# Optimization experiments

Hardware: AMD Instinct MI355X
Metric: run time of the kernel (lower is better)

## Reference

```python
import jax, jax.numpy as jnp
import numpy as np

EMBED = 1152
HEADS = 16
HEAD_DIM = EMBED // HEADS
SCALE = HEAD_DIM ** -0.5


def setup_inputs() -> dict:
    key = jax.random.key(0)
    k1, k2, k3, k4, k5 = jax.random.split(key, 5)
    B, S = 32, 729
    std = EMBED ** -0.5
    return {
        "hidden_state": jax.random.normal(k1, (B, S, EMBED), dtype=jnp.float32),
        "qkv_w": jax.random.normal(k2, (3 * EMBED, EMBED), dtype=jnp.float32) * std,
        "qkv_b": jax.random.normal(k3, (3 * EMBED,), dtype=jnp.float32) * 0.02,
        "out_w": jax.random.normal(k4, (EMBED, EMBED), dtype=jnp.float32) * std,
        "out_b": jax.random.normal(k5, (EMBED,), dtype=jnp.float32) * 0.02,
    }


def reference(hidden_state, qkv_w, qkv_b, out_w, out_b):
    B, S, _ = hidden_state.shape
    qkv = hidden_state @ qkv_w.T + qkv_b  # [B,S,3E]
    q, k, v = jnp.split(qkv, 3, axis=-1)
    # [B,S,E] -> [B,H,S,Dh]
    def heads(x):
        return x.reshape(B, S, HEADS, HEAD_DIM).transpose(0, 2, 1, 3)
    q, k, v = heads(q), heads(k), heads(v)
    scores = jnp.einsum("bhqd,bhkd->bhqk", q, k) * SCALE
    scores = jax.nn.softmax(scores, axis=-1)  # [B,H,S,S]
    out = jnp.einsum("bhqk,bhkd->bhqd", scores, v)
    out = out.transpose(0, 2, 1, 3).reshape(B, S, EMBED)
    out = out @ out_w.T + out_b
    return out, scores
```

## Files before the change

### kernel.cpp

```cpp
#include <hip/hip_runtime.h>

#define B_    32
#define S_    729
#define E_    1152
#define H_    16
#define D_    72
#define M1_   23328
#define MPAD_ 23424
#define SQ_   736
#define SK_   768
#define DP_   96
#define VR_   96
#define SCALE_ 0.11785113019775793f

typedef __attribute__((ext_vector_type(8))) _Float16 f16x8;
typedef __attribute__((ext_vector_type(4))) _Float16 f16x4;
typedef __attribute__((ext_vector_type(4))) float    f32x4;

#define GLDS16(g, l) __builtin_amdgcn_global_load_lds(                      \
    (__attribute__((address_space(1))) void*)(g),                           \
    (__attribute__((address_space(3))) void*)(l), 16, 0, 0)

union H2U { _Float16 h[2]; uint32_t u; };

__global__ void cvt_f16(const float4* __restrict__ src, f16x4* __restrict__ dst, int n4) {
  int stride = gridDim.x * blockDim.x;
  for (int i = blockIdx.x * blockDim.x + threadIdx.x; i < n4; i += stride) {
    float4 v = src[i];
    f16x4 o;
    o.x = (_Float16)v.x; o.y = (_Float16)v.y;
    o.z = (_Float16)v.z; o.w = (_Float16)v.w;
    dst[i] = o;
  }
}

template<int MODE>
__global__ __launch_bounds__(256)
void gemm_f16(const _Float16* __restrict__ A, const _Float16* __restrict__ W,
              const float* __restrict__ bias,
              _Float16* __restrict__ Qp, _Float16* __restrict__ Kp,
              _Float16* __restrict__ Vtp, float* __restrict__ Cout)
{
  __shared__ _Float16 As[128 * 64];
  __shared__ _Float16 Bs[128 * 64];
  const int tid = threadIdx.x;
  const int l  = tid & 63;
  const int wv = tid >> 6;
  const int lq = l & 15, lk = l >> 4;
  const int m0 = blockIdx.x * 128;
  const int n0 = blockIdx.y * 128;
  const int wm = (wv & 1) * 64, wn = (wv >> 1) * 64;
  const int srow = l >> 3;
  const int scol = (l & 7) * 8;

  f32x4 acc[4][4] = {};

  for (int k0 = 0; k0 < 1152; k0 += 64) {
    #pragma unroll
    for (int q = 0; q < 4; ++q) {
      int chunk = wv * 4 + q;
      int row = chunk * 8 + srow;
      GLDS16(A + (size_t)(m0 + row) * 1152 + k0 + scol, &As[chunk * 512 + l * 8]);
      GLDS16(W + (size_t)(n0 + row) * 1152 + k0 + scol, &Bs[chunk * 512 + l * 8]);
    }
    __syncthreads();
    #pragma unroll
    for (int kk = 0; kk < 64; kk += 32) {
      f16x8 a[4], b[4];
      #pragma unroll
      for (int i = 0; i < 4; ++i)
        a[i] = *(const f16x8*)&As[(wm + 16 * i + lq) * 64 + kk + lk * 8];
      #pragma unroll
      for (int j = 0; j < 4; ++j)
        b[j] = *(const f16x8*)&Bs[(wn + 16 * j + lq) * 64 + kk + lk * 8];
      #pragma unroll
      for (int i = 0; i < 4; ++i)
        #pragma unroll
        for (int j = 0; j < 4; ++j)
          acc[i][j] = __builtin_amdgcn_mfma_f32_16x16x32_f16(a[i], b[j], acc[i][j], 0, 0, 0);
    }
    __syncthreads();
  }

  #pragma unroll
  for (int i = 0; i < 4; ++i) {
    #pragma unroll
    for (int j = 0; j < 4; ++j) {
      int n = n0 + wn + 16 * j + lq;
      float bn = bias[n];
      #pragma unroll
      for (int r = 0; r < 4; ++r) {
        int m = m0 + wm + 16 * i + lk * 4 + r;
        if (m >= M1_) continue;
        float v = acc[i][j][r] + bn;
        if (MODE == 0) {
          unsigned um = (unsigned)m;
          unsigned bq = um / 729u, s = um - bq * 729u;
          unsigned un = (unsigned)n;
          unsigned which = un / 1152u, e = un - which * 1152u;
          unsigned h = e / 72u, d = e - h * 72u;
          unsigned bh = bq * 16u + h;
          if (which == 0) {
            Qp[((size_t)bh * SQ_ + s) * DP_ + d] = (_Float16)(v * SCALE_);
          } else if (which == 1) {
            Kp[((size_t)bh * SK_ + s) * DP_ + d] = (_Float16)v;
          } else {
            Vtp[((size_t)bh * VR_ + d) * 768 + s] = (_Float16)v;
          }
        } else {
          Cout[(size_t)m * 1152 + n] = v;
        }
      }
    }
  }
}

struct AttnSmem {
  union {
    char  stage[2][24576];
    float ored[4][32][96];
  };
  uint32_t pexch[8][64][4];
  float redmax[32][4];
  float redsum[32][4];
  float invl[32];
};

__global__ __launch_bounds__(512, 4)
void attn_k(const _Float16* __restrict__ Q, const _Float16* __restrict__ K,
            const _Float16* __restrict__ Vt, float* __restrict__ scores,
            _Float16* __restrict__ AO)
{
  __shared__ AttnSmem sm;
  const int tid = threadIdx.x;
  const int l   = tid & 63;
  const int wv  = tid >> 6;
  const int lq  = l & 15, lk = l >> 4;
  const int i   = wv >> 2;
  const int sl  = wv & 3;
  const int p    = blockIdx.x;
  const int xcd  = p & 7;
  const int slot = p >> 3;
  const int hl   = slot / 23;
  const int qt   = slot - hl * 23;
  const int bh   = hl * 8 + xcd;
  const int q0   = qt * 32;
  const int b    = bh >> 4, h = bh & 15;

  const _Float16* Qb = Q  + (size_t)bh * SQ_ * DP_;
  const _Float16* Kb = K  + (size_t)bh * SK_ * DP_;
  const _Float16* Vb = Vt + (size_t)bh * VR_ * 768;

  auto stage = [&](int idx) {
    char* buf = sm.stage[idx & 1];
    if (idx < 6) {
      #pragma unroll
      for (int it = 0; it < 3; ++it) {
        int s = it * 512 + tid;
        int row = s / 12, cp = s - row * 12;
        int cc = (cp < 8) ? (cp ^ (row & 7)) : (8 + ((cp & 3) ^ ((row >> 1) & 3)));
        GLDS16(Kb + (size_t)(idx * 128 + row) * DP_ + cc * 8, buf + s * 16);
      }
    } else {
      #pragma unroll
      for (int it = 0; it < 3; ++it) {
        int s = it * 512 + tid;
        int row = s >> 4, cp = s & 15;
        int cc = cp ^ (row & 15);
        GLDS16(Vb + (size_t)row * 768 + (idx - 6) * 128 + cc * 8, buf + s * 16);
      }
    }
  };

  stage(0);
  stage(1);
  f16x8 aq[3];
  {
    const _Float16* qp = Qb + (size_t)(q0 + 16 * i + lq) * DP_ + lk * 8;
    aq[0] = *(const f16x8*)(qp);
    aq[1] = *(const f16x8*)(qp + 32);
    aq[2] = *(const f16x8*)(qp + 64);
  }
  asm volatile("s_waitcnt vmcnt(0)" ::: "memory");
  __builtin_amdgcn_s_barrier();

  f32x4 sacc[12] = {};
  #pragma unroll
  for (int t = 0; t < 6; ++t) {
    asm volatile("s_waitcnt vmcnt(3)" ::: "memory");
    __builtin_amdgcn_s_barrier();
    const char* bufp = sm.stage[t & 1];
    #pragma unroll
    for (int lcb = 0; lcb < 2; ++lcb) {
      int row = (2 * sl + lcb) * 16 + lq;
      #pragma unroll
      for (int t3 = 0; t3 < 3; ++t3) {
        int cc = 4 * t3 + lk;
        int cp = (cc < 8) ? (cc ^ (row & 7)) : (8 + ((cc & 3) ^ ((row >> 1) & 3)));
        f16x8 ka = *(const f16x8*)(bufp + row * 192 + cp * 16);
        sacc[2 * t + lcb] = __builtin_amdgcn_mfma_f32_16x16x32_f16(ka, aq[t3], sacc[2 * t + lcb], 0, 0, 0);
      }
    }
    asm volatile("s_waitcnt lgkmcnt(0)" ::: "memory");
    __builtin_amdgcn_s_barrier();
    stage(t + 2);
  }

  #pragma unroll
  for (int c = 10; c < 12; ++c) {
    int kbase = (40 + 2 * sl + (c & 1)) * 16 + 4 * lk;
    #pragma unroll
    for (int r = 0; r < 4; ++r)
      if (kbase + r > 728) sacc[c][r] = -1e30f;
  }

  float m = -1e30f;
  #pragma unroll
  for (int c = 0; c < 12; ++c)
    #pragma unroll
    for (int r = 0; r < 4; ++r) m = fmaxf(m, sacc[c][r]);
  m = fmaxf(m, __shfl_xor(m, 16));
  m = fmaxf(m, __shfl_xor(m, 32));
  if (lk == 0) sm.redmax[16 * i + lq][sl] = m;
  asm volatile("s_waitcnt lgkmcnt(0)" ::: "memory");
  __builtin_amdgcn_s_barrier();
  float gm;
  { const float* rp = sm.redmax[16 * i + lq];
    gm = fmaxf(fmaxf(rp[0], rp[1]), fmaxf(rp[2], rp[3])); }

  float sum = 0.f;
  #pragma unroll
  for (int c = 0; c < 12; ++c)
    #pragma unroll
    for (int r = 0; r < 4; ++r) {
      float e = __expf(sacc[c][r] - gm);
      sacc[c][r] = e;
      sum += e;
    }
  sum += __shfl_xor(sum, 16);
  sum += __shfl_xor(sum, 32);
  if (lk == 0) sm.redsum[16 * i + lq][sl] = sum;
  asm volatile("s_waitcnt lgkmcnt(0)" ::: "memory");
  __builtin_amdgcn_s_barrier();
  float inv;
  { const float* rp = sm.redsum[16 * i + lq];
    inv = 1.0f / (rp[0] + rp[1] + rp[2] + rp[3]); }
  if (lk == 0 && sl == 0) sm.invl[16 * i + lq] = inv;

  uint32_t pk[12][2];
  #pragma unroll
  for (int c = 0; c < 12; ++c) {
    H2U a0, a1;
    a0.h[0] = (_Float16)sacc[c][0]; a0.h[1] = (_Float16)sacc[c][1];
    a1.h[0] = (_Float16)sacc[c][2]; a1.h[1] = (_Float16)sacc[c][3];
    pk[c][0] = a0.u; pk[c][1] = a1.u;
  }

  f32x4 oacc[6] = {};
  const int srcA = lq + 16 * (2 * (lk & 1));
  const int srcB = srcA + 16;
  #pragma unroll
  for (int v = 0; v < 6; ++v) {
    if (v < 5) { asm volatile("s_waitcnt vmcnt(3)" ::: "memory"); }
    else       { asm volatile("s_waitcnt vmcnt(0)" ::: "memory"); }
    __builtin_amdgcn_s_barrier();
    uint4 w = make_uint4(pk[2 * v][0], pk[2 * v][1], pk[2 * v + 1][0], pk[2 * v + 1][1]);
    *(uint4*)&sm.pexch[wv][l][0] = w;
    asm volatile("s_waitcnt lgkmcnt(0)" ::: "memory");
    __builtin_amdgcn_sched_barrier(0);
    uint2 dA = *(const uint2*)((const char*)&sm.pexch[wv][srcA][0] + (lk >> 1) * 8);
    uint2 dB = *(const uint2*)((const char*)&sm.pexch[wv][srcB][0] + (lk >> 1) * 8);
    uint4 pad4 = make_uint4(dA.x, dA.y, dB.x, dB.y);
    f16x8 pa = __builtin_bit_cast(f16x8, pad4);

    const char* bufp = sm.stage[v & 1];
    #pragma unroll
    for (int db = 0; db < 6; ++db) {
      int row = db * 16 + lq;
      int cc = 4 * sl + lk;
      int cp = cc ^ (row & 15);
      f16x8 bv = *(const f16x8*)(bufp + row * 256 + cp * 16);
      oacc[db] = __builtin_amdgcn_mfma_f32_16x16x32_f16(pa, bv, oacc[db], 0, 0, 0);
    }
    asm volatile("s_waitcnt lgkmcnt(0)" ::: "memory");
    __builtin_amdgcn_s_barrier();
    if (v < 4) stage(v + 8);
  }

  #pragma unroll
  for (int db = 0; db < 6; ++db)
    #pragma unroll
    for (int r = 0; r < 4; ++r) {
      int row = 16 * i + lk * 4 + r;
      sm.ored[sl][row][(db * 16 + lq) ^ (row & 12)] = oacc[db][r];
    }

  {
    const int q = q0 + 16 * i + lq;
    if (q < S_) {
      float* sc = scores + (size_t)bh * S_ * S_ + (size_t)q * S_;
      #pragma unroll
      for (int c = 0; c < 12; ++c) {
        int k0 = (8 * (c >> 1) + 2 * sl + (c & 1)) * 16 + 4 * lk;
        H2U u0, u1; u0.u = pk[c][0]; u1.u = pk[c][1];
        f32x4 vv;
        vv[0] = (float)u0.h[0] * inv; vv[1] = (float)u0.h[1] * inv;
        vv[2] = (float)u1.h[0] * inv; vv[3] = (float)u1.h[1] * inv;
        if (k0 + 3 <= 728)  *(f32x4*)(sc + k0) = vv;
        else if (k0 == 728) sc[728] = vv[0];
      }
    }
  }

  asm volatile("s_waitcnt lgkmcnt(0)" ::: "memory");
  __builtin_amdgcn_s_barrier();

  {
    int qq = tid >> 4, dc = tid & 15;
    int qglob = q0 + qq;
    if (dc < 12 && qglob < S_) {
      int d0 = dc * 6;
      float iv = sm.invl[qq];
      _Float16* ap = AO + ((size_t)(b * S_ + qglob)) * E_ + h * D_ + d0;
      #pragma unroll
      for (int e = 0; e < 6; ++e) {
        int col = (d0 + e) ^ (qq & 12);
        float v = sm.ored[0][qq][col] + sm.ored[1][qq][col]
                + sm.ored[2][qq][col] + sm.ored[3][qq][col];
        ap[e] = (_Float16)(v * iv);
      }
    }
  }
}

extern "C" void kernel_launch(void* const* d_in, const int* in_sizes, int n_in,
                              void* d_out, int out_size, void* d_ws, size_t ws_size,
                              hipStream_t stream)
{
  const float* hidden = (const float*)d_in[0];
  const float* qkv_w  = (const float*)d_in[1];
  const float* qkv_b  = (const float*)d_in[2];
  const float* out_w  = (const float*)d_in[3];
  const float* out_b  = (const float*)d_in[4];
  float* out    = (float*)d_out;
  float* scores = out + (size_t)M1_ * E_;

  char* ws = (char*)d_ws;
  const size_t szA1 = (size_t)MPAD_ * 1152 * 2;
  const size_t szWq = (size_t)3456 * 1152 * 2;
  const size_t szWo = (size_t)1152 * 1152 * 2;
  const size_t szQ  = (size_t)512 * SQ_ * DP_ * 2;
  const size_t szK  = (size_t)512 * SK_ * DP_ * 2;
  const size_t szV  = (size_t)512 * VR_ * 768 * 2;
  const size_t offA1 = 0;
  const size_t offWq = offA1 + szA1;
  const size_t offWo = offWq + szWq;
  const size_t offQ  = offWo + szWo;
  const size_t offK  = offQ  + szQ;
  const size_t offVt = offK  + szK;
  const size_t need  = offVt + szV;
  if (ws_size < need) return;

  _Float16* A1  = (_Float16*)(ws + offA1);
  _Float16* Wq  = (_Float16*)(ws + offWq);
  _Float16* Wo  = (_Float16*)(ws + offWo);
  _Float16* Qp  = (_Float16*)(ws + offQ);
  _Float16* Kp  = (_Float16*)(ws + offK);
  _Float16* Vtp = (_Float16*)(ws + offVt);
  _Float16* AO  = A1;

  hipMemsetAsync(Qp,  0, szQ, stream);
  hipMemsetAsync(Kp,  0, szK, stream);
  hipMemsetAsync(Vtp, 0, szV, stream);

  cvt_f16<<<26244, 256, 0, stream>>>((const float4*)hidden, (f16x4*)A1, (M1_ * E_) / 4);
  cvt_f16<<<3888,  256, 0, stream>>>((const float4*)qkv_w,  (f16x4*)Wq, (3456 * 1152) / 4);
  cvt_f16<<<1296,  256, 0, stream>>>((const float4*)out_w,  (f16x4*)Wo, (1152 * 1152) / 4);

  gemm_f16<0><<<dim3(183, 27), 256, 0, stream>>>(A1, Wq, qkv_b, Qp, Kp, Vtp, nullptr);
  attn_k<<<11776, 512, 0, stream>>>(Qp, Kp, Vtp, scores, AO);
  gemm_f16<1><<<dim3(183, 9), 256, 0, stream>>>(AO, Wo, out_b, nullptr, nullptr, nullptr, out);
}
```

Before: 1.174 ms.

## Stage softmax probabilities through LDS for coalesced score writes; fuse fp16 conversions

The attention kernel now writes the fp16 probabilities for each row into a swizzled LDS buffer. Each 16-thread group then reads its row back and writes the fp32 scores as contiguous 32-byte chunks, replacing the earlier scattered 16-byte per-lane global stores. This targets the large scores write, which is the dominant memory traffic. The three fp16 conversion launches are also merged into one grid-stride kernel with a fixed grid, removing launch overhead. The cost is extra barriers and LDS traffic in the attention kernel.

```diff
diff --git a/kernel.cpp b/kernel.cpp
--- a/kernel.cpp
+++ b/kernel.cpp
@@ -23,14 +23,24 @@
 
 union H2U { _Float16 h[2]; uint32_t u; };
 
-__global__ void cvt_f16(const float4* __restrict__ src, f16x4* __restrict__ dst, int n4) {
+#define N4H  6718464
+#define N4W1 995328
+#define N4W2 331776
+__global__ void cvt_all(const float4* __restrict__ hid, const float4* __restrict__ w1,
+                        const float4* __restrict__ w2, f16x4* __restrict__ o1,
+                        f16x4* __restrict__ o2, f16x4* __restrict__ o3) {
   int stride = gridDim.x * blockDim.x;
-  for (int i = blockIdx.x * blockDim.x + threadIdx.x; i < n4; i += stride) {
-    float4 v = src[i];
+  for (int i = blockIdx.x * blockDim.x + threadIdx.x;
+       i < N4H + N4W1 + N4W2; i += stride) {
+    const float4* s; f16x4* d; int j;
+    if (i < N4H)             { s = hid; d = o1; j = i; }
+    else if (i < N4H + N4W1) { s = w1;  d = o2; j = i - N4H; }
+    else                     { s = w2;  d = o3; j = i - N4H - N4W1; }
+    float4 v = s[j];
     f16x4 o;
     o.x = (_Float16)v.x; o.y = (_Float16)v.y;
     o.z = (_Float16)v.z; o.w = (_Float16)v.w;
-    dst[i] = o;
+    d[j] = o;
   }
 }
 
@@ -117,8 +127,9 @@
 
 struct AttnSmem {
   union {
-    char  stage[2][24576];
-    float ored[4][32][96];
+    char     stage[2][24576];
+    float    ored[4][32][96];
+    _Float16 p16[32][768];
   };
   uint32_t pexch[8][64][4];
   float redmax[32][4];
@@ -294,24 +305,6 @@
       int row = 16 * i + lk * 4 + r;
       sm.ored[sl][row][(db * 16 + lq) ^ (row & 12)] = oacc[db][r];
     }
-
-  {
-    const int q = q0 + 16 * i + lq;
-    if (q < S_) {
-      float* sc = scores + (size_t)bh * S_ * S_ + (size_t)q * S_;
-      #pragma unroll
-      for (int c = 0; c < 12; ++c) {
-        int k0 = (8 * (c >> 1) + 2 * sl + (c & 1)) * 16 + 4 * lk;
-        H2U u0, u1; u0.u = pk[c][0]; u1.u = pk[c][1];
-        f32x4 vv;
-        vv[0] = (float)u0.h[0] * inv; vv[1] = (float)u0.h[1] * inv;
-        vv[2] = (float)u1.h[0] * inv; vv[3] = (float)u1.h[1] * inv;
-        if (k0 + 3 <= 728)  *(f32x4*)(sc + k0) = vv;
-        else if (k0 == 728) sc[728] = vv[0];
-      }
-    }
-  }
-
   asm volatile("s_waitcnt lgkmcnt(0)" ::: "memory");
   __builtin_amdgcn_s_barrier();
 
@@ -328,6 +321,49 @@
         float v = sm.ored[0][qq][col] + sm.ored[1][qq][col]
                 + sm.ored[2][qq][col] + sm.ored[3][qq][col];
         ap[e] = (_Float16)(v * iv);
+      }
+    }
+  }
+  __builtin_amdgcn_s_barrier();
+
+  {
+    int row = 16 * i + lq;
+    char* base = (char*)sm.p16 + row * 1536;
+    #pragma unroll
+    for (int c = 0; c < 12; ++c) {
+      int cb = 8 * (c >> 1) + 2 * sl + (c & 1);
+      int off = cb * 32 + 8 * lk;
+      int swz = off ^ ((row & 7) << 4);
+      *(uint2*)(base + swz) = make_uint2(pk[c][0], pk[c][1]);
+    }
+  }
+  asm volatile("s_waitcnt lgkmcnt(0)" ::: "memory");
+  __builtin_amdgcn_s_barrier();
+
+  {
+    int row = tid >> 4;
+    int qg  = q0 + row;
+    if (qg < S_) {
+      float ivr = sm.invl[row];
+      float* srow = scores + (size_t)bh * S_ * S_ + (size_t)qg * S_;
+      const char* base = (const char*)sm.p16 + row * 1536;
+      #pragma unroll
+      for (int c6 = 0; c6 < 6; ++c6) {
+        int off = c6 * 256 + 16 * (tid & 15);
+        int swz = off ^ ((row & 7) << 4);
+        f16x8 pv8 = *(const f16x8*)(base + swz);
+        int k0 = c6 * 128 + 8 * (tid & 15);
+        f32x4 lo, hi;
+        lo[0] = (float)pv8[0] * ivr; lo[1] = (float)pv8[1] * ivr;
+        lo[2] = (float)pv8[2] * ivr; lo[3] = (float)pv8[3] * ivr;
+        hi[0] = (float)pv8[4] * ivr; hi[1] = (float)pv8[5] * ivr;
+        hi[2] = (float)pv8[6] * ivr; hi[3] = (float)pv8[7] * ivr;
+        if (k0 + 7 <= 728) {
+          *(f32x4*)(srow + k0)     = lo;
+          *(f32x4*)(srow + k0 + 4) = hi;
+        } else if (k0 == 728) {
+          srow[728] = lo[0];
+        }
       }
     }
   }
@@ -373,9 +409,9 @@
   hipMemsetAsync(Kp,  0, szK, stream);
   hipMemsetAsync(Vtp, 0, szV, stream);
 
-  cvt_f16<<<26244, 256, 0, stream>>>((const float4*)hidden, (f16x4*)A1, (M1_ * E_) / 4);
-  cvt_f16<<<3888,  256, 0, stream>>>((const float4*)qkv_w,  (f16x4*)Wq, (3456 * 1152) / 4);
-  cvt_f16<<<1296,  256, 0, stream>>>((const float4*)out_w,  (f16x4*)Wo, (1152 * 1152) / 4);
+  cvt_all<<<2048, 256, 0, stream>>>((const float4*)hidden, (const float4*)qkv_w,
+                                    (const float4*)out_w, (f16x4*)A1,
+                                    (f16x4*)Wq, (f16x4*)Wo);
 
   gemm_f16<0><<<dim3(183, 27), 256, 0, stream>>>(A1, Wq, qkv_b, Qp, Kp, Vtp, nullptr);
   attn_k<<<11776, 512, 0, stream>>>(Qp, Kp, Vtp, scores, AO);
```

New measurement: 1.257 ms. 1.07x slower.
